# Kernel optimization log

Hardware: AMD Instinct MI355X
Metric: run time of the kernel (lower is better)

Reference implementation:

```python
import jax, jax.numpy as jnp
import numpy as np

B, S, D_IN = 2, 2048, 2048
H, G, HD = 16, 4, 128          # heads, kv groups, head_dim
GS = H // G                    # group size (heads per kv group)
EPS = 1e-6
SCALE = HD ** -0.5


def rms_norm(x, w):
    # RMSNorm over last dim (head_dim)
    var = jnp.mean(jnp.square(x), axis=-1, keepdims=True)
    return x * jax.lax.rsqrt(var + EPS) * w


def apply_rope(x, cos, sin):
    # x: [b, h, s, d]; cos/sin: [s, d]. Rotate-half convention.
    d = x.shape[-1]
    x1, x2 = x[..., : d // 2], x[..., d // 2 :]
    rotated = jnp.concatenate([-x2, x1], axis=-1)
    return x * cos[None, None] + rotated * sin[None, None]


def setup_inputs() -> dict:
    key = jax.random.key(0)
    ks = jax.random.split(key, 8)
    x = jax.random.normal(ks[0], (B, S, D_IN), jnp.float32)
    mask = jnp.triu(jnp.ones((S, S), jnp.bool_), k=1)  # True = masked (future)
    # realistic RoPE tables
    inv_freq = 1.0 / (10000.0 ** (jnp.arange(0, HD, 2, dtype=jnp.float32) / HD))
    angles = jnp.arange(S, dtype=jnp.float32)[:, None] * inv_freq[None, :]  # [S, HD/2]
    angles = jnp.concatenate([angles, angles], axis=-1)  # [S, HD]
    cos, sin = jnp.cos(angles), jnp.sin(angles)
    sd = 0.02
    Wq = jax.random.normal(ks[1], (D_IN, H * HD), jnp.float32) * sd
    Wk = jax.random.normal(ks[2], (D_IN, G * HD), jnp.float32) * sd
    Wv = jax.random.normal(ks[3], (D_IN, G * HD), jnp.float32) * sd
    Wo = jax.random.normal(ks[4], (H * HD, D_IN), jnp.float32) * sd
    q_norm_w = jnp.ones((HD,), jnp.float32)
    k_norm_w = jnp.ones((HD,), jnp.float32)
    return {"x": x, "mask": mask, "cos": cos, "sin": sin, "Wq": Wq, "Wk": Wk,
            "Wv": Wv, "Wo": Wo, "q_norm_w": q_norm_w, "k_norm_w": k_norm_w}


def reference(x, mask, cos, sin, Wq, Wk, Wv, Wo, q_norm_w, k_norm_w):
    b, s, _ = x.shape
    q = (x @ Wq).reshape(b, s, H, HD).transpose(0, 2, 1, 3)   # [b,H,s,d]
    k = (x @ Wk).reshape(b, s, G, HD).transpose(0, 2, 1, 3)   # [b,G,s,d]
    v = (x @ Wv).reshape(b, s, G, HD).transpose(0, 2, 1, 3)   # [b,G,s,d]
    q = rms_norm(q, q_norm_w)
    k = rms_norm(k, k_norm_w)
    q = apply_rope(q, cos, sin)
    k = apply_rope(k, cos, sin)
    q = q * SCALE
    # GQA without materializing repeated KV: split heads into [G, GS]
    qg = q.reshape(b, G, GS, s, HD)                           # [b,G,gs,s,d]
    scores = jnp.einsum('bghsd,bgtd->bghst', qg, k)           # [b,G,gs,s,s]
    scores = jnp.where(mask[None, None, None], -jnp.inf, scores)
    attn = jax.nn.softmax(scores, axis=-1)
    ctx = jnp.einsum('bghst,bgtd->bghsd', attn, v)            # [b,G,gs,s,d]
    ctx = ctx.reshape(b, H, s, HD).transpose(0, 2, 1, 3).reshape(b, s, H * HD)
    return ctx @ Wo
```

## Files before the change

kernel.cpp:

```cpp
#include <hip/hip_runtime.h>
#include <cstdint>
#include <cstddef>

typedef unsigned short u16;
typedef __bf16 bf16x8 __attribute__((ext_vector_type(8)));
typedef float f32x4 __attribute__((ext_vector_type(4)));

#define SLEN 2048
#define NHEADS 16
#define NGRP 4

__device__ inline float bf2f(u16 u) { return __uint_as_float(((unsigned)u) << 16); }
__device__ inline u16 f2bf(float f) {
    unsigned u = __float_as_uint(f);
    u += 0x7fffu + ((u >> 16) & 1u);
    return (u16)(u >> 16);
}

__device__ inline f32x4 mfma16(bf16x8 a, bf16x8 b, f32x4 c) {
    return __builtin_amdgcn_mfma_f32_16x16x32_bf16(a, b, c, 0, 0, 0);
}

__device__ inline void memfence_compiler() { __asm__ volatile("" ::: "memory"); }

__device__ inline void cp16(const u16* g, u16* l) {
    __builtin_amdgcn_global_load_lds(
        (__attribute__((address_space(1))) void*)(u16*)g,
        (__attribute__((address_space(3))) void*)l, 16, 0, 0);
}

__global__ __launch_bounds__(256) void convert_k(const float* __restrict__ in, u16* __restrict__ out,
                                                 long n) {
    long i = ((long)blockIdx.x * 256 + threadIdx.x) * 4;
    if (i >= n) return;
    float4 v = *(const float4*)(in + i);
    ushort4 o;
    o.x = f2bf(v.x); o.y = f2bf(v.y); o.z = f2bf(v.z); o.w = f2bf(v.w);
    *(ushort4*)(out + i) = o;
}

__global__ __launch_bounds__(128) void convert_small_k(const float* __restrict__ qw,
                                                       const float* __restrict__ kw,
                                                       u16* qwb, u16* kwb) {
    int t = threadIdx.x;
    qwb[t] = f2bf(qw[t]);
    kwb[t] = f2bf(kw[t]);
}

__global__ __launch_bounds__(256) void transpose_f32_k(const float* __restrict__ in,
                                                       u16* __restrict__ out, int R, int C) {
    __shared__ u16 tile[64][65];
    const int tid = threadIdx.x;
    const long r0 = (long)blockIdx.y * 64, c0 = (long)blockIdx.x * 64;
    for (int j = 0; j < 4; j++) {
        int c = j * 256 + tid;
        int lr = c >> 4, lc = (c & 15) * 4;
        float4 v = *(const float4*)&in[(r0 + lr) * (long)C + c0 + lc];
        tile[lr][lc + 0] = f2bf(v.x); tile[lr][lc + 1] = f2bf(v.y);
        tile[lr][lc + 2] = f2bf(v.z); tile[lr][lc + 3] = f2bf(v.w);
    }
    __syncthreads();
    for (int j = 0; j < 4; j++) {
        int c = j * 256 + tid;
        int orow = c >> 4, oc = (c & 15) * 4;
        ushort4 vv;
        vv.x = tile[oc + 0][orow]; vv.y = tile[oc + 1][orow];
        vv.z = tile[oc + 2][orow]; vv.w = tile[oc + 3][orow];
        *(ushort4*)&out[(c0 + orow) * (long)R + r0 + oc] = vv;
    }
}

__global__ __launch_bounds__(256) void transpose_bf_k(const u16* __restrict__ in, long inRS,
                                                      u16* __restrict__ out, int R, int C) {
    __shared__ u16 tile[64][65];
    const int tid = threadIdx.x;
    const long r0 = (long)blockIdx.y * 64, c0 = (long)blockIdx.x * 64;
    for (int j = 0; j < 4; j++) {
        int c = j * 256 + tid;
        int lr = c >> 4, lc = (c & 15) * 4;
        ushort4 vv = *(const ushort4*)&in[(r0 + lr) * inRS + c0 + lc];
        tile[lr][lc + 0] = vv.x; tile[lr][lc + 1] = vv.y;
        tile[lr][lc + 2] = vv.z; tile[lr][lc + 3] = vv.w;
    }
    __syncthreads();
    for (int j = 0; j < 4; j++) {
        int c = j * 256 + tid;
        int orow = c >> 4, oc = (c & 15) * 4;
        ushort4 vv;
        vv.x = tile[oc + 0][orow]; vv.y = tile[oc + 1][orow];
        vv.z = tile[oc + 2][orow]; vv.w = tile[oc + 3][orow];
        *(ushort4*)&out[(c0 + orow) * (long)R + r0 + oc] = vv;
    }
}

template <typename OutT>
__global__ __launch_bounds__(256) void gemm_bt(const u16* __restrict__ A, const u16* __restrict__ Bt,
                                               OutT* __restrict__ C, int M, int N, int K) {
    __shared__ u16 As[128 * 32];
    __shared__ u16 Bs[128 * 32];
    const int tid = threadIdx.x;
    const int lane = tid & 63, wave = tid >> 6;
    const int l15 = lane & 15, quad = lane >> 4;
    const long m0 = (long)blockIdx.y * 128, n0 = (long)blockIdx.x * 128;
    const int wm = (wave >> 1) * 64, wn = (wave & 1) * 64;

    f32x4 acc[4][4];
    for (int i = 0; i < 4; i++)
        for (int j = 0; j < 4; j++) acc[i][j] = {0.f, 0.f, 0.f, 0.f};

    const u16* aG = A + (m0 + wave * 32 + (lane >> 2)) * (long)K + (lane & 3) * 8;
    const u16* bG = Bt + (n0 + wave * 32 + (lane >> 2)) * (long)K + (lane & 3) * 8;
    u16* aL = &As[wave * 1024];
    u16* bL = &Bs[wave * 1024];
    const long rowK16 = 16L * K;

    for (int kt = 0; kt < K; kt += 32) {
        cp16(aG + kt, aL);
        cp16(aG + kt + rowK16, aL + 512);
        cp16(bG + kt, bL);
        cp16(bG + kt + rowK16, bL + 512);
        __syncthreads();
        bf16x8 af[4], bfr[4];
        for (int mi = 0; mi < 4; mi++)
            af[mi] = *(const bf16x8*)&As[(wm + mi * 16 + l15) * 32 + quad * 8];
        for (int ni = 0; ni < 4; ni++)
            bfr[ni] = *(const bf16x8*)&Bs[(wn + ni * 16 + l15) * 32 + quad * 8];
        for (int mi = 0; mi < 4; mi++)
            for (int ni = 0; ni < 4; ni++)
                acc[mi][ni] = mfma16(af[mi], bfr[ni], acc[mi][ni]);
        __syncthreads();
    }
    for (int mi = 0; mi < 4; mi++)
        for (int r = 0; r < 4; r++) {
            long row = m0 + wm + mi * 16 + quad * 4 + r;
            OutT* crow = C + row * (long)N + n0 + wn + l15;
            for (int ni = 0; ni < 4; ni++) {
                float v = acc[mi][ni][r];
                if constexpr (sizeof(OutT) == 2) crow[ni * 16] = f2bf(v);
                else crow[ni * 16] = v;
            }
        }
}

__global__ __launch_bounds__(256) void normrope(u16* __restrict__ buf, long rowstride, int heads,
                                                const u16* __restrict__ w,
                                                const float* __restrict__ cosf, const float* __restrict__ sinf,
                                                float scale) {
    const int row = blockIdx.x * 4 + (threadIdx.x >> 6);
    const int lane = threadIdx.x & 63;
    u16* p = buf + (long)(row / heads) * rowstride + (row % heads) * 128;
    float x1 = bf2f(p[lane]);
    float x2 = bf2f(p[lane + 64]);
    float ss = x1 * x1 + x2 * x2;
    for (int off = 1; off < 64; off <<= 1) ss += __shfl_xor(ss, off);
    float inv = rsqrtf(ss * (1.f / 128.f) + 1e-6f);
    int s = (row / heads) % SLEN;
    float c1 = cosf[s * 128 + lane], c2 = cosf[s * 128 + 64 + lane];
    float s1 = sinf[s * 128 + lane], s2 = sinf[s * 128 + 64 + lane];
    float w1 = bf2f(w[lane]), w2 = bf2f(w[lane + 64]);
    float y1 = x1 * inv * w1, y2 = x2 * inv * w2;
    p[lane]      = f2bf((y1 * c1 - y2 * s1) * scale);
    p[lane + 64] = f2bf((y2 * c2 + y1 * s2) * scale);
}

__global__ __launch_bounds__(256, 2) void attn(const u16* __restrict__ qkv, const u16* __restrict__ vT,
                                               u16* __restrict__ ctx) {
    __shared__ u16 KB[64 * 128];
    __shared__ u16 VB[128 * 64];
    __shared__ u16 Ps[4][2][16][72];
    __shared__ float Al[4][2][16];
    const int tid = threadIdx.x;
    const int lane = tid & 63, wave = tid >> 6;
    const int l15 = lane & 15, quad = lane >> 4;
    const int bg = blockIdx.x & 7, b = bg >> 2, g = bg & 3;
    const int rest = blockIdx.x >> 3;
    const int h = g * 4 + (rest & 3);
    const int idx = rest >> 2;
    const int qt = (idx < 8) ? (15 - idx) : (idx - 8);
    const int wr = qt * 128 + wave * 32;

    union { bf16x8 v; u16 s[8]; } uo;
    for (int j = 0; j < 8; j++) uo.s[j] = 0x3F80;
    const bf16x8 ones = uo.v;

    bf16x8 qa[2][4];
    for (int m = 0; m < 2; m++) {
        const u16* qp = qkv + (long)(b * SLEN + wr + m * 16 + l15) * 3072 + h * 128 + quad * 8;
        for (int kc = 0; kc < 4; kc++) qa[m][kc] = *(const bf16x8*)(qp + kc * 32);
    }
    float m_i[2] = {-__builtin_inff(), -__builtin_inff()};
    f32x4 l_acc[2];
    f32x4 o[2][8];
    for (int m = 0; m < 2; m++) l_acc[m] = {0.f, 0.f, 0.f, 0.f};
    for (int m = 0; m < 2; m++)
        for (int nf = 0; nf < 8; nf++) o[m][nf] = {0.f, 0.f, 0.f, 0.f};

    const u16* kqb = qkv + (long)b * SLEN * 3072 + 2048 + g * 128;
    const u16* vgb = vT + (long)g * 128 * 4096 + (long)b * SLEN;
    const int xk = (l15 & 7) << 4;
    const int nt = 2 * qt + 2;

    for (int t = 0; t < nt; ++t) {
        const int t0 = t * 64;
        #pragma unroll
        for (int i = 0; i < 4; ++i) {
            const int j = wave * 4 + i;
            {
                const int row = j * 4 + (lane >> 4);
                const int cs = lane & 15;
                cp16(kqb + (long)(t0 + row) * 3072 + ((cs ^ (row & 7)) * 8), &KB[j * 512]);
            }
            {
                const int row = j * 8 + (lane >> 3);
                const int cs = lane & 7;
                cp16(vgb + (long)row * 4096 + t0 + ((cs ^ (row & 7)) * 8), &VB[j * 512]);
            }
        }
        __syncthreads();

        if (t0 <= wr + 31) {
            bf16x8 kf[4][4];
            #pragma unroll
            for (int nf = 0; nf < 4; nf++)
                #pragma unroll
                for (int kc = 0; kc < 4; kc++)
                    kf[nf][kc] = *(const bf16x8*)((const char*)KB +
                                  (nf * 16 + l15) * 256 + ((quad * 16 + kc * 64) ^ xk));

            f32x4 sc[2][4];
            for (int m = 0; m < 2; m++)
                for (int nf = 0; nf < 4; nf++) sc[m][nf] = {0.f, 0.f, 0.f, 0.f};
            #pragma unroll
            for (int kc = 0; kc < 4; kc++)
                #pragma unroll
                for (int nf = 0; nf < 4; nf++) {
                    sc[0][nf] = mfma16(kf[nf][kc], qa[0][kc], sc[0][nf]);
                    sc[1][nf] = mfma16(kf[nf][kc], qa[1][kc], sc[1][nf]);
                }
            if (t0 + 63 > wr) {
                #pragma unroll
                for (int m = 0; m < 2; m++) {
                    int qrow = wr + m * 16 + l15;
                    #pragma unroll
                    for (int nf = 0; nf < 4; nf++)
                        #pragma unroll
                        for (int r = 0; r < 4; r++)
                            if (t0 + nf * 16 + quad * 4 + r > qrow) sc[m][nf][r] = -__builtin_inff();
                }
            }
            float alpha[2];
            #pragma unroll
            for (int m = 0; m < 2; m++) {
                float mx = sc[m][0][0];
                #pragma unroll
                for (int nf = 0; nf < 4; nf++)
                    #pragma unroll
                    for (int r = 0; r < 4; r++) mx = fmaxf(mx, sc[m][nf][r]);
                mx = fmaxf(mx, __shfl_xor(mx, 16));
                mx = fmaxf(mx, __shfl_xor(mx, 32));
                float mn = fmaxf(m_i[m], mx);
                alpha[m] = __expf(m_i[m] - mn);
                m_i[m] = mn;
                Al[wave][m][l15] = alpha[m];
            }
            #pragma unroll
            for (int m = 0; m < 2; m++)
                #pragma unroll
                for (int nf = 0; nf < 4; nf++) {
                    ushort4 pk;
                    pk.x = f2bf(__expf(sc[m][nf][0] - m_i[m]));
                    pk.y = f2bf(__expf(sc[m][nf][1] - m_i[m]));
                    pk.z = f2bf(__expf(sc[m][nf][2] - m_i[m]));
                    pk.w = f2bf(__expf(sc[m][nf][3] - m_i[m]));
                    *(ushort4*)&Ps[wave][m][l15][nf * 16 + quad * 4] = pk;
                }
            memfence_compiler();
            f32x4 al[2];
            al[0] = *(const f32x4*)&Al[wave][0][quad * 4];
            al[1] = *(const f32x4*)&Al[wave][1][quad * 4];
            #pragma unroll
            for (int m = 0; m < 2; m++) {
                #pragma unroll
                for (int nf = 0; nf < 8; nf++)
                    #pragma unroll
                    for (int r = 0; r < 4; r++) o[m][nf][r] *= al[m][r];
                #pragma unroll
                for (int r = 0; r < 4; r++) l_acc[m][r] *= al[m][r];
            }
            {
                bf16x8 vf[8];
                #pragma unroll
                for (int nf = 0; nf < 8; nf++)
                    vf[nf] = *(const bf16x8*)((const char*)VB +
                              (nf * 16 + l15) * 128 + ((quad * 16) ^ xk));
                bf16x8 pa0 = *(const bf16x8*)&Ps[wave][0][l15][quad * 8];
                bf16x8 pa1 = *(const bf16x8*)&Ps[wave][1][l15][quad * 8];
                #pragma unroll
                for (int nf = 0; nf < 8; nf++) {
                    o[0][nf] = mfma16(pa0, vf[nf], o[0][nf]);
                    o[1][nf] = mfma16(pa1, vf[nf], o[1][nf]);
                }
                l_acc[0] = mfma16(pa0, ones, l_acc[0]);
                l_acc[1] = mfma16(pa1, ones, l_acc[1]);
            }
            {
                bf16x8 vf[8];
                #pragma unroll
                for (int nf = 0; nf < 8; nf++)
                    vf[nf] = *(const bf16x8*)((const char*)VB +
                              (nf * 16 + l15) * 128 + ((64 + quad * 16) ^ xk));
                bf16x8 pa0 = *(const bf16x8*)&Ps[wave][0][l15][32 + quad * 8];
                bf16x8 pa1 = *(const bf16x8*)&Ps[wave][1][l15][32 + quad * 8];
                #pragma unroll
                for (int nf = 0; nf < 8; nf++) {
                    o[0][nf] = mfma16(pa0, vf[nf], o[0][nf]);
                    o[1][nf] = mfma16(pa1, vf[nf], o[1][nf]);
                }
                l_acc[0] = mfma16(pa0, ones, l_acc[0]);
                l_acc[1] = mfma16(pa1, ones, l_acc[1]);
            }
            memfence_compiler();
        }
        __syncthreads();
    }

    #pragma unroll
    for (int m = 0; m < 2; m++)
        #pragma unroll
        for (int r = 0; r < 4; r++) {
            float inv = 1.f / l_acc[m][r];
            int srow = wr + m * 16 + quad * 4 + r;
            u16* cp = ctx + (long)(b * SLEN + srow) * 2048 + h * 128 + l15;
            #pragma unroll
            for (int nf = 0; nf < 8; nf++) cp[nf * 16] = f2bf(o[m][nf][r] * inv);
        }
}

extern "C" void kernel_launch(void* const* d_in, const int* in_sizes, int n_in,
                              void* d_out, int out_size, void* d_ws, size_t ws_size,
                              hipStream_t stream) {
    const float* x    = (const float*)d_in[0];
    const float* cosi = (const float*)d_in[2];
    const float* sini = (const float*)d_in[3];
    const float* Wq   = (const float*)d_in[4];
    const float* Wk   = (const float*)d_in[5];
    const float* Wv   = (const float*)d_in[6];
    const float* Wo   = (const float*)d_in[7];
    const float* qw   = (const float*)d_in[8];
    const float* kw   = (const float*)d_in[9];
    float* out = (float*)d_out;
    char* ws = (char*)d_ws;

    const size_t MB = 1 << 20;
    u16* qkvb  = (u16*)(ws);
    u16* vTb   = (u16*)(ws + 24 * MB);
    u16* xbf   = (u16*)(ws + 28 * MB);
    u16* ctx   = (u16*)(ws + 28 * MB);
    u16* wqkvT = (u16*)(ws + 44 * MB);
    u16* woT   = (u16*)(ws + 44 * MB);
    u16* qwb   = (u16*)(ws + 56 * MB);
    u16* kwb   = (u16*)(ws + 56 * MB + 256);

    convert_k<<<8192, 256, 0, stream>>>(x, xbf, 8388608L);
    convert_small_k<<<1, 128, 0, stream>>>(qw, kw, qwb, kwb);

    transpose_f32_k<<<dim3(32, 32), 256, 0, stream>>>(Wq, wqkvT, 2048, 2048);
    transpose_f32_k<<<dim3(8, 32), 256, 0, stream>>>(Wk, wqkvT + 2048L * 2048, 2048, 512);
    transpose_f32_k<<<dim3(8, 32), 256, 0, stream>>>(Wv, wqkvT + 2560L * 2048, 2048, 512);

    gemm_bt<u16><<<dim3(24, 32), 256, 0, stream>>>(xbf, wqkvT, qkvb, 4096, 3072, 2048);

    transpose_bf_k<<<dim3(8, 64), 256, 0, stream>>>(qkvb + 2560, 3072L, vTb, 4096, 512);

    normrope<<<16384, 256, 0, stream>>>(qkvb, 3072L, NHEADS, qwb, cosi, sini, 0.08838834764831845f);
    normrope<<<4096, 256, 0, stream>>>(qkvb + 2048, 3072L, NGRP, kwb, cosi, sini, 1.0f);

    transpose_f32_k<<<dim3(32, 32), 256, 0, stream>>>(Wo, woT, 2048, 2048);

    attn<<<dim3(512, 1, 1), 256, 0, stream>>>(qkvb, vTb, ctx);

    gemm_bt<float><<<dim3(16, 32), 256, 0, stream>>>(ctx, woT, out, 4096, 2048, 2048);
}
```

Measured before the change: 364.2 us.

## Replace 128x128 GEMM with double-buffered swizzled 256x256 tile kernel

Replaces the single-buffered 128x128 bf16 GEMM with a 512-thread kernel that computes 256x256 output tiles over a K-step of 64. LDS is double-buffered (128KB dynamic shared memory), and the next stage is prefetched while the current one is consumed, with explicit vmcnt waits. An XOR swizzle on the LDS layout avoids bank conflicts. The aim is more data reuse per load and overlap of global loads with MFMA work. In exchange the grids shrink to 192 and 128 blocks, which may leave many CUs idle, and the large LDS footprint limits occupancy.

```diff
diff --git a/kernel.cpp b/kernel.cpp
--- a/kernel.cpp
+++ b/kernel.cpp
@@ -94,46 +94,92 @@
 }
 
 template <typename OutT>
-__global__ __launch_bounds__(256) void gemm_bt(const u16* __restrict__ A, const u16* __restrict__ Bt,
-                                               OutT* __restrict__ C, int M, int N, int K) {
-    __shared__ u16 As[128 * 32];
-    __shared__ u16 Bs[128 * 32];
+__global__ __launch_bounds__(512, 2) void gemm256(const u16* __restrict__ A, const u16* __restrict__ Bt,
+                                                  OutT* __restrict__ C, int N, int K) {
+    extern __shared__ u16 smem[];
     const int tid = threadIdx.x;
     const int lane = tid & 63, wave = tid >> 6;
     const int l15 = lane & 15, quad = lane >> 4;
-    const long m0 = (long)blockIdx.y * 128, n0 = (long)blockIdx.x * 128;
-    const int wm = (wave >> 1) * 64, wn = (wave & 1) * 64;
-
-    f32x4 acc[4][4];
-    for (int i = 0; i < 4; i++)
+    const int wm = (wave >> 2) * 128, wn = (wave & 3) * 64;
+    const long m0 = (long)blockIdx.y * 256, n0 = (long)blockIdx.x * 256;
+
+    f32x4 acc[8][4];
+    #pragma unroll
+    for (int i = 0; i < 8; i++)
+        #pragma unroll
         for (int j = 0; j < 4; j++) acc[i][j] = {0.f, 0.f, 0.f, 0.f};
 
-    const u16* aG = A + (m0 + wave * 32 + (lane >> 2)) * (long)K + (lane & 3) * 8;
-    const u16* bG = Bt + (n0 + wave * 32 + (lane >> 2)) * (long)K + (lane & 3) * 8;
-    u16* aL = &As[wave * 1024];
-    u16* bL = &Bs[wave * 1024];
-    const long rowK16 = 16L * K;
-
-    for (int kt = 0; kt < K; kt += 32) {
-        cp16(aG + kt, aL);
-        cp16(aG + kt + rowK16, aL + 512);
-        cp16(bG + kt, bL);
-        cp16(bG + kt + rowK16, bL + 512);
-        __syncthreads();
-        bf16x8 af[4], bfr[4];
-        for (int mi = 0; mi < 4; mi++)
-            af[mi] = *(const bf16x8*)&As[(wm + mi * 16 + l15) * 32 + quad * 8];
-        for (int ni = 0; ni < 4; ni++)
-            bfr[ni] = *(const bf16x8*)&Bs[(wn + ni * 16 + l15) * 32 + quad * 8];
-        for (int mi = 0; mi < 4; mi++)
-            for (int ni = 0; ni < 4; ni++)
-                acc[mi][ni] = mfma16(af[mi], bfr[ni], acc[mi][ni]);
-        __syncthreads();
-    }
-    for (int mi = 0; mi < 4; mi++)
+    const int sn = wave * 64 + lane;
+    const u16* aBase = A + m0 * (long)K;
+    const u16* bBase = Bt + n0 * (long)K;
+
+    auto stage = [&](int kt, int p) {
+        u16* al = smem + p * 16384 + wave * 512;
+        u16* bl = smem + 32768 + p * 16384 + wave * 512;
+        #pragma unroll
+        for (int j = 0; j < 4; j++) {
+            int n = j * 512 + sn;
+            int r = n >> 3;
+            int c = (n & 7) ^ (r & 7);
+            cp16(aBase + (long)r * K + kt + c * 8, al + j * 4096);
+            cp16(bBase + (long)r * K + kt + c * 8, bl + j * 4096);
+        }
+    };
+
+    stage(0, 0);
+    const int nkt = K >> 6;
+
+    for (int t = 0; t < nkt; ++t) {
+        const int cur = t & 1;
+        if (t + 1 < nkt) {
+            stage((t + 1) << 6, cur ^ 1);
+            asm volatile("s_waitcnt vmcnt(8)" ::: "memory");
+        } else {
+            asm volatile("s_waitcnt vmcnt(0)" ::: "memory");
+        }
+        __builtin_amdgcn_s_barrier();
+
+        const u16* asb = smem + cur * 16384;
+        const u16* bsb = smem + 32768 + cur * 16384;
+
+        bf16x8 bfr[4][2];
+        #pragma unroll
+        for (int ni = 0; ni < 4; ni++) {
+            const int row = wn + ni * 16 + l15;
+            #pragma unroll
+            for (int ks = 0; ks < 2; ks++)
+                bfr[ni][ks] = *(const bf16x8*)&bsb[row * 64 + (((ks << 2) + quad) ^ (row & 7)) * 8];
+        }
+        #pragma unroll
+        for (int mq = 0; mq < 2; mq++) {
+            bf16x8 af[4][2];
+            #pragma unroll
+            for (int mi = 0; mi < 4; mi++) {
+                const int row = wm + mq * 64 + mi * 16 + l15;
+                #pragma unroll
+                for (int ks = 0; ks < 2; ks++)
+                    af[mi][ks] = *(const bf16x8*)&asb[row * 64 + (((ks << 2) + quad) ^ (row & 7)) * 8];
+            }
+            #pragma unroll
+            for (int mi = 0; mi < 4; mi++)
+                #pragma unroll
+                for (int ni = 0; ni < 4; ni++) {
+                    f32x4 v = acc[mq * 4 + mi][ni];
+                    v = mfma16(af[mi][0], bfr[ni][0], v);
+                    v = mfma16(af[mi][1], bfr[ni][1], v);
+                    acc[mq * 4 + mi][ni] = v;
+                }
+        }
+        __builtin_amdgcn_s_barrier();
+    }
+
+    #pragma unroll
+    for (int mi = 0; mi < 8; mi++)
+        #pragma unroll
         for (int r = 0; r < 4; r++) {
             long row = m0 + wm + mi * 16 + quad * 4 + r;
             OutT* crow = C + row * (long)N + n0 + wn + l15;
+            #pragma unroll
             for (int ni = 0; ni < 4; ni++) {
                 float v = acc[mi][ni][r];
                 if constexpr (sizeof(OutT) == 2) crow[ni * 16] = f2bf(v);
@@ -274,7 +320,7 @@
                     pk.w = f2bf(__expf(sc[m][nf][3] - m_i[m]));
                     *(ushort4*)&Ps[wave][m][l15][nf * 16 + quad * 4] = pk;
                 }
-            memfence_compiler();
+        memfence_compiler();
             f32x4 al[2];
             al[0] = *(const f32x4*)&Al[wave][0][quad * 4];
             al[1] = *(const f32x4*)&Al[wave][1][quad * 4];
@@ -368,7 +414,7 @@
     transpose_f32_k<<<dim3(8, 32), 256, 0, stream>>>(Wk, wqkvT + 2048L * 2048, 2048, 512);
     transpose_f32_k<<<dim3(8, 32), 256, 0, stream>>>(Wv, wqkvT + 2560L * 2048, 2048, 512);
 
-    gemm_bt<u16><<<dim3(24, 32), 256, 0, stream>>>(xbf, wqkvT, qkvb, 4096, 3072, 2048);
+    gemm256<u16><<<dim3(12, 16), 512, 131072, stream>>>(xbf, wqkvT, qkvb, 3072, 2048);
 
     transpose_bf_k<<<dim3(8, 64), 256, 0, stream>>>(qkvb + 2560, 3072L, vTb, 4096, 512);
 
@@ -379,5 +425,5 @@
 
     attn<<<dim3(512, 1, 1), 256, 0, stream>>>(qkvb, vTb, ctx);
 
-    gemm_bt<float><<<dim3(16, 32), 256, 0, stream>>>(ctx, woT, out, 4096, 2048, 2048);
-}
+    gemm256<float><<<dim3(8, 16), 512, 131072, stream>>>(ctx, woT, out, 2048, 2048);
+}
```

Result: faster. 354.4 us (-2.7%).
